# Kernel tuning notes

Hardware: AMD Instinct MI355X
Metric: run time of the kernel (lower is better)

## Reference

```python
import jax, jax.numpy as jnp
import numpy as np

DIM = 1024
NUM_HEADS = 16
HEAD_DIM = DIM // NUM_HEADS
SCALE = HEAD_DIM ** -0.5


def setup_inputs() -> dict:
    key = jax.random.key(0)
    k_x, k_qkv, k_proj, k_pb = jax.random.split(key, 4)
    B, N = 4, 2048
    x = jax.random.normal(k_x, (B, N, DIM), dtype=jnp.float32)
    # qkv: Linear(dim, 3*dim), qkv_bias=False -> no bias
    W_qkv = jax.random.normal(k_qkv, (DIM, 3 * DIM), dtype=jnp.float32) * (DIM ** -0.5)
    # proj: Linear(dim, dim) with bias (nn.Linear default)
    W_proj = jax.random.normal(k_proj, (DIM, DIM), dtype=jnp.float32) * (DIM ** -0.5)
    b_proj = jax.random.normal(k_pb, (DIM,), dtype=jnp.float32) * 0.01
    return {"x": x, "W_qkv": W_qkv, "W_proj": W_proj, "b_proj": b_proj}


def reference(x, W_qkv, W_proj, b_proj):
    B, N, C = x.shape
    H, D = NUM_HEADS, HEAD_DIM
    # qkv projection -> [B, N, 3, H, D] -> q,k,v each [B, H, N, D]
    qkv = (x @ W_qkv).reshape(B, N, 3, H, D)
    q, k, v = (jnp.moveaxis(qkv, 2, 0).transpose(0, 1, 3, 2, 4))  # [3,B,H,N,D]
    # attention scores [B, H, N, N], scaled QK^T (full matrix, as in source)
    attn = jnp.einsum('bhqd,bhkd->bhqk', q, k) * SCALE
    attn = jax.nn.softmax(attn, axis=-1)
    # attn @ V -> [B, H, N, D] -> [B, N, C]
    out = jnp.einsum('bhqk,bhkd->bhqd', attn, v)
    out = out.transpose(0, 2, 1, 3).reshape(B, N, C)
    # output projection
    return out @ W_proj + b_proj
```

## Files before the change

kernel.cpp:

```cpp
#include <hip/hip_runtime.h>
#include <hip/hip_bf16.h>

typedef __attribute__((ext_vector_type(8))) short short8;
typedef __attribute__((ext_vector_type(4))) short short4_t;
typedef __attribute__((ext_vector_type(4))) float floatx4;
typedef unsigned short u16;
typedef unsigned int u32;

#define SEQ 2048
#define NH 16
#define HD 64
#define CDIM 1024
#define MTOT 8192

__device__ __forceinline__ u16 f2bf(float f) {
  u32 u = __builtin_bit_cast(u32, f);
  u32 r = u + 0x7FFFu + ((u >> 16) & 1u);
  return (u16)(r >> 16);
}

__device__ __forceinline__ void gload16(const void* g, void* l) {
  __builtin_amdgcn_global_load_lds(
      (const __attribute__((address_space(1))) u32*)g,
      (__attribute__((address_space(3))) u32*)l, 16, 0, 0);
}

__global__ void prep_all(const float* __restrict__ x, u16* __restrict__ xb,
                         const float* __restrict__ Wqkv, u16* __restrict__ wqkvT,
                         const float* __restrict__ Wproj, u16* __restrict__ wprojT) {
  int bid = blockIdx.x;
  if (bid < 4096) {
    size_t i = (size_t)bid * 256 + threadIdx.x;
    const float4* xv = (const float4*)x;
    float4 a = xv[2 * i], c = xv[2 * i + 1];
    union { u16 h[8]; short8 v; } u;
    u.h[0] = f2bf(a.x); u.h[1] = f2bf(a.y); u.h[2] = f2bf(a.z); u.h[3] = f2bf(a.w);
    u.h[4] = f2bf(c.x); u.h[5] = f2bf(c.y); u.h[6] = f2bf(c.z); u.h[7] = f2bf(c.w);
    *(short8*)(xb + 8 * i) = u.v;
    return;
  }
  __shared__ float t[32][33];
  const float* w; u16* wt; int N, nb, kb;
  if (bid < 7168) { int tt = bid - 4096; w = Wqkv; wt = wqkvT; N = 3072; nb = tt % 96; kb = tt / 96; }
  else            { int tt = bid - 7168; w = Wproj; wt = wprojT; N = 1024; nb = tt % 32; kb = tt / 32; }
  const int K = 1024;
  int n0 = nb * 32, k0 = kb * 32;
  int tr = threadIdx.x >> 5, tc = threadIdx.x & 31;
#pragma unroll
  for (int i = 0; i < 4; i++) {
    int r = tr + i * 8;
    t[r][tc] = w[(size_t)(k0 + r) * N + n0 + tc];
  }
  __syncthreads();
#pragma unroll
  for (int i = 0; i < 4; i++) {
    int r = tr + i * 8;
    wt[(size_t)(n0 + r) * K + k0 + tc] = f2bf(t[tc][r]);
  }
}

__global__ __launch_bounds__(256, 2) void gemm_qkv(
    const u16* __restrict__ A, const u16* __restrict__ BT,
    u16* __restrict__ qb, u16* __restrict__ kb, u16* __restrict__ vtb) {
  __shared__ u16 Ab[128 * 64];
  __shared__ u16 Bb[128 * 64];
  const int tid = threadIdx.x;
  const int w = tid >> 6, l = tid & 63;
  const int quad = l >> 4, l15 = l & 15;
  const int m0 = blockIdx.x * 128, n0 = blockIdx.y * 128;
  const int wr = w >> 1, wc = w & 1;

  floatx4 acc[4][4] = {};

  for (int k0 = 0; k0 < 1024; k0 += 64) {
    __syncthreads();
#pragma unroll
    for (int rnd = 0; rnd < 4; rnd++) {
      int ci = rnd * 256 + tid;
      int r = ci >> 3, pos = ci & 7;
      int c = pos ^ (r & 7);
      gload16(A + (size_t)(m0 + r) * 1024 + k0 + c * 8, (char*)Ab + ci * 16);
      gload16(BT + (size_t)(n0 + r) * 1024 + k0 + c * 8, (char*)Bb + ci * 16);
    }
    __syncthreads();
    short8 af[4][2], bf[4][2];
#pragma unroll
    for (int t = 0; t < 4; t++) {
      int ra = wr * 64 + t * 16 + l15;
      int ga = ra & 7;
#pragma unroll
      for (int ks = 0; ks < 2; ks++)
        af[t][ks] = *(short8*)((char*)Ab + ra * 128 + ((ks * 4 + quad) ^ ga) * 16);
      int rb = wc * 64 + t * 16 + l15;
      int gb = rb & 7;
#pragma unroll
      for (int ks = 0; ks < 2; ks++)
        bf[t][ks] = *(short8*)((char*)Bb + rb * 128 + ((ks * 4 + quad) ^ gb) * 16);
    }
#pragma unroll
    for (int ks = 0; ks < 2; ks++)
#pragma unroll
      for (int i = 0; i < 4; i++)
#pragma unroll
        for (int j = 0; j < 4; j++)
          acc[i][j] = __builtin_amdgcn_mfma_f32_16x16x32_bf16(af[i][ks], bf[j][ks], acc[i][j], 0, 0, 0);
  }

#pragma unroll
  for (int i = 0; i < 4; i++)
#pragma unroll
    for (int j = 0; j < 4; j++)
#pragma unroll
      for (int r = 0; r < 4; r++) {
        int m = m0 + wr * 64 + i * 16 + quad * 4 + r;
        int c = n0 + wc * 64 + j * 16 + l15;
        int b = m >> 11, n = m & 2047;
        int t = c >> 10, rem = c & 1023;
        int h = rem >> 6, d = rem & 63;
        int bh = b * NH + h;
        if (t == 0)      qb[((size_t)bh * SEQ + n) * HD + d] = f2bf(acc[i][j][r] * 0.18033688011112042f);
        else if (t == 1) kb[((size_t)bh * SEQ + n) * HD + d] = f2bf(acc[i][j][r]);
        else             vtb[((size_t)bh * HD + d) * SEQ + n] = f2bf(acc[i][j][r]);
      }
}

__global__ __launch_bounds__(256, 2) void gemm_proj(
    const u16* __restrict__ A, const u16* __restrict__ BT,
    const float* __restrict__ bias, float* __restrict__ out) {
  __shared__ u16 Ab[128 * 64];
  __shared__ u16 Bb[128 * 64];
  const int tid = threadIdx.x;
  const int w = tid >> 6, l = tid & 63;
  const int quad = l >> 4, l15 = l & 15;
  const int m0 = blockIdx.x * 128, n0 = blockIdx.y * 128;
  const int wr = w >> 1, wc = w & 1;

  floatx4 acc[4][4] = {};

  for (int k0 = 0; k0 < 1024; k0 += 64) {
    __syncthreads();
#pragma unroll
    for (int rnd = 0; rnd < 4; rnd++) {
      int ci = rnd * 256 + tid;
      int r = ci >> 3, pos = ci & 7;
      int c = pos ^ (r & 7);
      gload16(A + (size_t)(m0 + r) * 1024 + k0 + c * 8, (char*)Ab + ci * 16);
      gload16(BT + (size_t)(n0 + r) * 1024 + k0 + c * 8, (char*)Bb + ci * 16);
    }
    __syncthreads();
    short8 af[4][2], bf[4][2];
#pragma unroll
    for (int t = 0; t < 4; t++) {
      int ra = wr * 64 + t * 16 + l15;
      int ga = ra & 7;
#pragma unroll
      for (int ks = 0; ks < 2; ks++)
        af[t][ks] = *(short8*)((char*)Ab + ra * 128 + ((ks * 4 + quad) ^ ga) * 16);
      int rb = wc * 64 + t * 16 + l15;
      int gb = rb & 7;
#pragma unroll
      for (int ks = 0; ks < 2; ks++)
        bf[t][ks] = *(short8*)((char*)Bb + rb * 128 + ((ks * 4 + quad) ^ gb) * 16);
    }
#pragma unroll
    for (int ks = 0; ks < 2; ks++)
#pragma unroll
      for (int i = 0; i < 4; i++)
#pragma unroll
        for (int j = 0; j < 4; j++)
          acc[i][j] = __builtin_amdgcn_mfma_f32_16x16x32_bf16(af[i][ks], bf[j][ks], acc[i][j], 0, 0, 0);
  }

#pragma unroll
  for (int i = 0; i < 4; i++)
#pragma unroll
    for (int j = 0; j < 4; j++)
#pragma unroll
      for (int r = 0; r < 4; r++) {
        int m = m0 + wr * 64 + i * 16 + quad * 4 + r;
        int c = n0 + wc * 64 + j * 16 + l15;
        out[(size_t)m * CDIM + c] = acc[i][j][r] + bias[c];
      }
}

__global__ __launch_bounds__(256, 2) void attn_kernel(
    const u16* __restrict__ Qb, const u16* __restrict__ Kb,
    const u16* __restrict__ Vtb, u16* __restrict__ attnb) {
  __shared__ char smem[65536];
  const int tid = threadIdx.x;
  const int w = tid >> 6, l = tid & 63;
  const int quad = l >> 4, l15 = l & 15;

  const int lb = blockIdx.x + (blockIdx.y << 3);
  const int bh = ((lb & 7) << 3) + ((lb >> 3) & 7);
  const int qt0 = (lb >> 6) * 256;

  const u16* Kbase = Kb + (size_t)bh * SEQ * HD;
  const u16* Vbase = Vtb + (size_t)bh * HD * SEQ;

  short8 qf[4][2];
#pragma unroll
  for (int rt = 0; rt < 4; rt++) {
    int qrow = qt0 + w * 64 + rt * 16 + l15;
#pragma unroll
    for (int ks = 0; ks < 2; ks++)
      qf[rt][ks] = *(const short8*)(Qb + ((size_t)bh * SEQ + qrow) * HD + ks * 32 + quad * 8);
  }

  floatx4 O[4][4] = {};
  floatx4 sumacc[4] = {};

  union { u16 h[8]; short8 v; } onesu;
#pragma unroll
  for (int z = 0; z < 8; z++) onesu.h[z] = 0x3F80;
  const short8 ones = onesu.v;

  auto stage = [&](int n0, char* base) {
#pragma unroll
    for (int rnd = 0; rnd < 4; rnd++) {
      int ci = rnd * 256 + tid;
      int r = ci >> 3, pos = ci & 7;
      int c = pos ^ ((r & 7) ^ ((r >> 1) & 4));
      gload16(Kbase + (size_t)(n0 + r) * HD + c * 8, base + ci * 16);
    }
#pragma unroll
    for (int rnd = 0; rnd < 4; rnd++) {
      int ci = rnd * 256 + tid;
      int r = ci >> 4, pos = ci & 15;
      int c = pos ^ (r & 15);
      gload16(Vbase + (size_t)r * SEQ + n0 + c * 8, base + 16384 + ci * 16);
    }
  };

  stage(0, smem);
  __syncthreads();

  for (int kt = 0; kt < 16; kt++) {
    char* cur = smem + (kt & 1) * 32768;
    if (kt < 15) stage((kt + 1) * 128, smem + ((kt + 1) & 1) * 32768);

    char* KtC = cur;
    char* VtsC = cur + 16384;
#pragma unroll
    for (int p = 0; p < 4; p++) {
      floatx4 s[2][4];
#pragma unroll
      for (int t = 0; t < 2; t++) {
        int rho = p * 32 + (l15 >> 2) * 8 + t * 4 + (l15 & 3);
        int g = (rho & 7) ^ ((rho >> 1) & 4);
        short8 kf0 = *(short8*)(KtC + rho * 128 + ((0 + quad) ^ g) * 16);
        short8 kf1 = *(short8*)(KtC + rho * 128 + ((4 + quad) ^ g) * 16);
#pragma unroll
        for (int rt = 0; rt < 4; rt++) {
          floatx4 z = {};
          z = __builtin_amdgcn_mfma_f32_16x16x32_bf16(kf0, qf[rt][0], z, 0, 0, 0);
          z = __builtin_amdgcn_mfma_f32_16x16x32_bf16(kf1, qf[rt][1], z, 0, 0, 0);
          s[t][rt] = z;
        }
      }
      short8 pf[4];
#pragma unroll
      for (int rt = 0; rt < 4; rt++) {
        union { u32 d[4]; short8 v; } pu;
#pragma unroll
        for (int t = 0; t < 2; t++) {
          float e0 = __builtin_amdgcn_exp2f(s[t][rt][0]);
          float e1 = __builtin_amdgcn_exp2f(s[t][rt][1]);
          float e2 = __builtin_amdgcn_exp2f(s[t][rt][2]);
          float e3 = __builtin_amdgcn_exp2f(s[t][rt][3]);
          pu.d[t * 2 + 0] = __builtin_amdgcn_perm(
              __builtin_bit_cast(u32, e1), __builtin_bit_cast(u32, e0), 0x07060302u);
          pu.d[t * 2 + 1] = __builtin_amdgcn_perm(
              __builtin_bit_cast(u32, e3), __builtin_bit_cast(u32, e2), 0x07060302u);
        }
        pf[rt] = pu.v;
        sumacc[rt] = __builtin_amdgcn_mfma_f32_16x16x32_bf16(ones, pf[rt], sumacc[rt], 0, 0, 0);
      }
#pragma unroll
      for (int dt = 0; dt < 4; dt++) {
        int rv = dt * 16 + l15;
        short8 vf = *(short8*)(VtsC + rv * 256 + ((p * 4 + quad) ^ (rv & 15)) * 16);
#pragma unroll
        for (int rt = 0; rt < 4; rt++)
          O[rt][dt] = __builtin_amdgcn_mfma_f32_16x16x32_bf16(vf, pf[rt], O[rt][dt], 0, 0, 0);
      }
    }
    __syncthreads();
  }

  float inv[4];
#pragma unroll
  for (int rt = 0; rt < 4; rt++) inv[rt] = 1.f / sumacc[rt][0];

#pragma unroll
  for (int rt = 0; rt < 4; rt++)
#pragma unroll
    for (int dt = 0; dt < 4; dt++) {
      union { u16 h[4]; short4_t v; } pk;
#pragma unroll
      for (int r = 0; r < 4; r++) pk.h[r] = f2bf(O[rt][dt][r] * inv[rt]);
      *(short4_t*)(smem + (w * 64 + rt * 16 + l15) * 144 + (dt * 16 + quad * 4) * 2) = pk.v;
    }
  __syncthreads();
  {
    const int b = bh >> 4, h = bh & 15;
#pragma unroll
    for (int it = 0; it < 2; it++) {
      int row = it * 128 + (tid >> 1);
      int half = tid & 1;
      u16* gp = attnb + ((size_t)(b * SEQ + qt0 + row)) * CDIM + h * 64 + half * 32;
      char* lp = smem + row * 144 + half * 64;
#pragma unroll
      for (int c = 0; c < 4; c++)
        *(short8*)(gp + c * 8) = *(short8*)(lp + c * 16);
    }
  }
}

extern "C" void kernel_launch(void* const* d_in, const int* in_sizes, int n_in,
                              void* d_out, int out_size, void* d_ws, size_t ws_size,
                              hipStream_t stream) {
  const float* x = (const float*)d_in[0];
  const float* Wqkv = (const float*)d_in[1];
  const float* Wproj = (const float*)d_in[2];
  const float* bproj = (const float*)d_in[3];
  float* out = (float*)d_out;

  u16* xb = (u16*)d_ws;
  u16* wqkvT = xb + (size_t)8388608;
  u16* wprojT = wqkvT + (size_t)3145728;
  u16* qb = wprojT + (size_t)1048576;
  u16* kb = qb + (size_t)8388608;
  u16* vtb = kb + (size_t)8388608;
  u16* attnb = xb;

  prep_all<<<8192, 256, 0, stream>>>(x, xb, Wqkv, wqkvT, Wproj, wprojT);
  gemm_qkv<<<dim3(64, 24), 256, 0, stream>>>(xb, wqkvT, qb, kb, vtb);
  attn_kernel<<<dim3(8, 64), 256, 0, stream>>>(qb, kb, vtb, attnb);
  gemm_proj<<<dim3(64, 8), 256, 0, stream>>>(attnb, wprojT, bproj, out);
}
```

Baseline: 252.7 us.

## Switch attention inner loop from 16x16x32 to 32x32x16 MFMA tiles

Rewrites the attention kernel's QK^T, row-sum and PV matrix multiplies to use 32x32x16 bf16 MFMA instructions instead of 16x16x32. Each wave now holds two 32-row query tiles and two 32-column head-dim tiles, with a permuted K row mapping so the score output layout feeds straight into the P operand. Larger MFMA tiles raise operand reuse per LDS fragment load and cut instruction count. In exchange the lane/register mapping changes throughout, and the epilogue write layout has to be redone to match.

Result: no change. 249.1 us (-1.4%).

```diff
diff --git a/kernel.cpp b/kernel.cpp
--- a/kernel.cpp
+++ b/kernel.cpp
@@ -4,6 +4,7 @@
 typedef __attribute__((ext_vector_type(8))) short short8;
 typedef __attribute__((ext_vector_type(4))) short short4_t;
 typedef __attribute__((ext_vector_type(4))) float floatx4;
+typedef __attribute__((ext_vector_type(16))) float floatx16;
 typedef unsigned short u16;
 typedef unsigned int u32;
 
@@ -189,7 +190,7 @@
   __shared__ char smem[65536];
   const int tid = threadIdx.x;
   const int w = tid >> 6, l = tid & 63;
-  const int quad = l >> 4, l15 = l & 15;
+  const int l31 = l & 31, hA = l >> 5;
 
   const int lb = blockIdx.x + (blockIdx.y << 3);
   const int bh = ((lb & 7) << 3) + ((lb >> 3) & 7);
@@ -198,17 +199,19 @@
   const u16* Kbase = Kb + (size_t)bh * SEQ * HD;
   const u16* Vbase = Vtb + (size_t)bh * HD * SEQ;
 
-  short8 qf[4][2];
-#pragma unroll
-  for (int rt = 0; rt < 4; rt++) {
-    int qrow = qt0 + w * 64 + rt * 16 + l15;
-#pragma unroll
-    for (int ks = 0; ks < 2; ks++)
-      qf[rt][ks] = *(const short8*)(Qb + ((size_t)bh * SEQ + qrow) * HD + ks * 32 + quad * 8);
-  }
-
-  floatx4 O[4][4] = {};
-  floatx4 sumacc[4] = {};
+  const int krow_perm = (l31 & 19) | ((l31 & 4) << 1) | ((l31 & 8) >> 1);
+
+  short8 qf[2][4];
+#pragma unroll
+  for (int qtile = 0; qtile < 2; qtile++) {
+    int qrow = qt0 + w * 64 + qtile * 32 + l31;
+#pragma unroll
+    for (int ks = 0; ks < 4; ks++)
+      qf[qtile][ks] = *(const short8*)(Qb + ((size_t)bh * SEQ + qrow) * HD + ks * 16 + hA * 8);
+  }
+
+  floatx16 O[2][2] = {};
+  floatx16 sumacc[2] = {};
 
   union { u16 h[8]; short8 v; } onesu;
 #pragma unroll
@@ -243,64 +246,66 @@
     char* VtsC = cur + 16384;
 #pragma unroll
     for (int p = 0; p < 4; p++) {
-      floatx4 s[2][4];
-#pragma unroll
-      for (int t = 0; t < 2; t++) {
-        int rho = p * 32 + (l15 >> 2) * 8 + t * 4 + (l15 & 3);
-        int g = (rho & 7) ^ ((rho >> 1) & 4);
-        short8 kf0 = *(short8*)(KtC + rho * 128 + ((0 + quad) ^ g) * 16);
-        short8 kf1 = *(short8*)(KtC + rho * 128 + ((4 + quad) ^ g) * 16);
-#pragma unroll
-        for (int rt = 0; rt < 4; rt++) {
-          floatx4 z = {};
-          z = __builtin_amdgcn_mfma_f32_16x16x32_bf16(kf0, qf[rt][0], z, 0, 0, 0);
-          z = __builtin_amdgcn_mfma_f32_16x16x32_bf16(kf1, qf[rt][1], z, 0, 0, 0);
-          s[t][rt] = z;
+      short8 kf[4];
+      {
+        int krow = p * 32 + krow_perm;
+        int gK = (krow & 7) ^ ((krow >> 1) & 4);
+#pragma unroll
+        for (int ks = 0; ks < 4; ks++)
+          kf[ks] = *(short8*)(KtC + krow * 128 + ((2 * ks + hA) ^ gK) * 16);
+      }
+      short8 pf[2][2];
+#pragma unroll
+      for (int qtile = 0; qtile < 2; qtile++) {
+        floatx16 s = {};
+#pragma unroll
+        for (int ks = 0; ks < 4; ks++)
+          s = __builtin_amdgcn_mfma_f32_32x32x16_bf16(kf[ks], qf[qtile][ks], s, 0, 0, 0);
+#pragma unroll
+        for (int t = 0; t < 2; t++) {
+          union { u32 d[4]; short8 v; } pu;
+#pragma unroll
+          for (int jj = 0; jj < 4; jj++) {
+            float ea = __builtin_amdgcn_exp2f(s[8 * t + 2 * jj]);
+            float eb = __builtin_amdgcn_exp2f(s[8 * t + 2 * jj + 1]);
+            pu.d[jj] = __builtin_amdgcn_perm(
+                __builtin_bit_cast(u32, eb), __builtin_bit_cast(u32, ea), 0x07060302u);
+          }
+          pf[qtile][t] = pu.v;
+          sumacc[qtile] = __builtin_amdgcn_mfma_f32_32x32x16_bf16(ones, pf[qtile][t], sumacc[qtile], 0, 0, 0);
         }
       }
-      short8 pf[4];
-#pragma unroll
-      for (int rt = 0; rt < 4; rt++) {
-        union { u32 d[4]; short8 v; } pu;
+#pragma unroll
+      for (int dt = 0; dt < 2; dt++) {
+        int rv = dt * 32 + l31;
 #pragma unroll
         for (int t = 0; t < 2; t++) {
-          float e0 = __builtin_amdgcn_exp2f(s[t][rt][0]);
-          float e1 = __builtin_amdgcn_exp2f(s[t][rt][1]);
-          float e2 = __builtin_amdgcn_exp2f(s[t][rt][2]);
-          float e3 = __builtin_amdgcn_exp2f(s[t][rt][3]);
-          pu.d[t * 2 + 0] = __builtin_amdgcn_perm(
-              __builtin_bit_cast(u32, e1), __builtin_bit_cast(u32, e0), 0x07060302u);
-          pu.d[t * 2 + 1] = __builtin_amdgcn_perm(
-              __builtin_bit_cast(u32, e3), __builtin_bit_cast(u32, e2), 0x07060302u);
+          short8 vf = *(short8*)(VtsC + rv * 256 + ((p * 4 + 2 * t + hA) ^ (rv & 15)) * 16);
+#pragma unroll
+          for (int qtile = 0; qtile < 2; qtile++)
+            O[qtile][dt] = __builtin_amdgcn_mfma_f32_32x32x16_bf16(vf, pf[qtile][t], O[qtile][dt], 0, 0, 0);
         }
-        pf[rt] = pu.v;
-        sumacc[rt] = __builtin_amdgcn_mfma_f32_16x16x32_bf16(ones, pf[rt], sumacc[rt], 0, 0, 0);
-      }
-#pragma unroll
-      for (int dt = 0; dt < 4; dt++) {
-        int rv = dt * 16 + l15;
-        short8 vf = *(short8*)(VtsC + rv * 256 + ((p * 4 + quad) ^ (rv & 15)) * 16);
-#pragma unroll
-        for (int rt = 0; rt < 4; rt++)
-          O[rt][dt] = __builtin_amdgcn_mfma_f32_16x16x32_bf16(vf, pf[rt], O[rt][dt], 0, 0, 0);
-      }
-    }
-    __syncthreads();
-  }
-
-  float inv[4];
-#pragma unroll
-  for (int rt = 0; rt < 4; rt++) inv[rt] = 1.f / sumacc[rt][0];
-
-#pragma unroll
-  for (int rt = 0; rt < 4; rt++)
-#pragma unroll
-    for (int dt = 0; dt < 4; dt++) {
-      union { u16 h[4]; short4_t v; } pk;
-#pragma unroll
-      for (int r = 0; r < 4; r++) pk.h[r] = f2bf(O[rt][dt][r] * inv[rt]);
-      *(short4_t*)(smem + (w * 64 + rt * 16 + l15) * 144 + (dt * 16 + quad * 4) * 2) = pk.v;
-    }
+      }
+    }
+    __syncthreads();
+  }
+
+  float inv[2] = {1.f / sumacc[0][0], 1.f / sumacc[1][0]};
+
+#pragma unroll
+  for (int qtile = 0; qtile < 2; qtile++) {
+    int qloc = w * 64 + qtile * 32 + l31;
+#pragma unroll
+    for (int dt = 0; dt < 2; dt++)
+#pragma unroll
+      for (int rg = 0; rg < 4; rg++) {
+        union { u16 h[4]; short4_t v; } pk;
+#pragma unroll
+        for (int i = 0; i < 4; i++) pk.h[i] = f2bf(O[qtile][dt][rg * 4 + i] * inv[qtile]);
+        int dbase = dt * 32 + rg * 8 + 4 * hA;
+        *(short4_t*)(smem + qloc * 144 + dbase * 2) = pk.v;
+      }
+  }
   __syncthreads();
   {
     const int b = bh >> 4, h = bh & 15;
```
